# Kernel tuning notes

Hardware: AMD Instinct MI355X
Metric: run time of the kernel (lower is better)

## Reference

```python
import jax, jax.numpy as jnp
import numpy as np

N_NODES = 50000
N_EDGES = 600000
D_IN = 128
D_OUT = 128
K_HOPS = 2  # Gra_inc(2)


def _gcn_norm(edge_index, edge_weight, num_nodes, dtype):
    # Add self-loops (weight 1.0) and compute symmetric GCN normalization.
    loop = jnp.arange(num_nodes, dtype=edge_index.dtype)
    row = jnp.concatenate([edge_index[0], loop])  # source
    col = jnp.concatenate([edge_index[1], loop])  # destination
    w = jnp.concatenate([edge_weight, jnp.ones((num_nodes,), dtype=dtype)])
    deg = jax.ops.segment_sum(w, col, num_segments=num_nodes)
    dinv = jnp.where(deg > 0, jax.lax.rsqrt(deg), jnp.zeros_like(deg))
    norm = dinv[row] * w * dinv[col]  # [E + N]
    return row, col, norm


def setup_inputs() -> dict:
    key = jax.random.key(0)
    k1, k2, k3, k4 = jax.random.split(key, 4)
    x = jax.random.normal(k1, (N_NODES, D_IN), dtype=jnp.float32)
    edge_index = jax.random.randint(k2, (2, N_EDGES), 0, N_NODES, dtype=jnp.int64)
    edge_weight = jax.random.uniform(k3, (N_EDGES,), dtype=jnp.float32)
    # Linear(in,out,bias=False) weight, PyTorch layout [out, in]
    W = jax.random.normal(k4, (D_OUT, D_IN), dtype=jnp.float32) * (1.0 / np.sqrt(D_IN))
    return {"x": x, "edge_index": edge_index, "edge_weight": edge_weight, "W": W}


def reference(x, edge_index, edge_weight, W):
    num_nodes = x.shape[0]
    h = x @ W.T  # lin11: [N, D_OUT]
    row, col, norm = _gcn_norm(edge_index, edge_weight, num_nodes, h.dtype)
    # Gra_inc(2): K=2 hops of normalized sparse propagation h <- A_hat @ h
    for _ in range(K_HOPS):
        msgs = norm[:, None] * h[row]  # gather + scale, [E+N, D_OUT]
        h = jax.ops.segment_sum(msgs, col, num_segments=num_nodes)
    return h  # bias is None (bias=False)
```

## Files before the change

kernel.cpp:

```cpp
#include <hip/hip_runtime.h>

typedef unsigned long long u64;
typedef unsigned int u32;
typedef _Float16 f16;

#define NN 50000
#define NE 600000
#define D  128
#define NWAVE 3125
#define GGEMM 782
#define EPB 2048
#define NB_P 293
#define NP 196
#define MAXCAP 3584
#define NSTRIP 2
#define GS 1563

typedef __attribute__((ext_vector_type(8))) __bf16 bf16x8;
typedef __attribute__((ext_vector_type(8))) unsigned short us8;
typedef __attribute__((ext_vector_type(8))) f16 f16x8;
typedef __attribute__((ext_vector_type(4))) float f32x4;

__device__ __forceinline__ unsigned short f2bf(float f) {
    u32 u = __float_as_uint(f);
    return (unsigned short)((u + 0x7FFFu + ((u >> 16) & 1u)) >> 16);
}
__device__ __forceinline__ float bf2f(unsigned short h) {
    return __uint_as_float((u32)h << 16);
}

__global__ __launch_bounds__(256) void wprep(const float* __restrict__ W,
                                             us8* __restrict__ Whi,
                                             us8* __restrict__ Wlo,
                                             int* __restrict__ pcur) {
    const int i = blockIdx.x * 256 + threadIdx.x;
    if (i < NP) pcur[i] = i * MAXCAP;
    if (i < 2048) {
        const int ln = i & 63, nt = (i >> 6) & 7, kc4 = i >> 9;
        const float* p =
            W + (size_t)(nt * 16 + (ln & 15)) * D + kc4 * 32 + (ln >> 4) * 8;
        float v[8];
        *(float4*)&v[0] = *(const float4*)p;
        *(float4*)&v[4] = *(const float4*)(p + 4);
        us8 hi, lo;
#pragma unroll
        for (int j = 0; j < 8; ++j) {
            const unsigned short hb = f2bf(v[j]);
            hi[j] = hb;
            lo[j] = f2bf(v[j] - bf2f(hb));
        }
        Whi[i] = hi;
        Wlo[i] = lo;
    }
}

__global__ __launch_bounds__(256) void gemm_scatter(
    const float* __restrict__ x, const us8* __restrict__ Whi,
    const us8* __restrict__ Wlo, f16* __restrict__ h16,
    const int* __restrict__ row, const int* __restrict__ col,
    const float* __restrict__ w, int* __restrict__ pcur,
    u64* __restrict__ part) {
    const int t = threadIdx.x;
    __shared__ us8 WH[2048];
    __shared__ us8 WL[2048];

    if (blockIdx.x < NB_P) {
        int* bins = (int*)WH;
        int* off0 = bins + 256;
        int* cur  = off0 + 256;
        for (int i = t; i < NP; i += 256) { bins[i] = 0; cur[i] = 0; }
        __syncthreads();
        const int e0 = blockIdx.x * EPB + t;
        int cc[8];
#pragma unroll
        for (int s = 0; s < 8; ++s) {
            const int e = e0 + s * 256;
            cc[s] = (e < NE) ? col[e] : -1;
            if (cc[s] >= 0) atomicAdd(&bins[cc[s] >> 8], 1);
        }
        __syncthreads();
        for (int i = t; i < NP; i += 256)
            off0[i] = bins[i] ? atomicAdd(&pcur[i], bins[i]) : 0;
        __syncthreads();
#pragma unroll
        for (int s = 0; s < 8; ++s) {
            const int e = e0 + s * 256;
            if (e < NE) {
                const int c = cc[s];
                const int p = c >> 8;
                const int lr = atomicAdd(&cur[p], 1);
                part[off0[p] + lr] = ((u64)__float_as_uint(w[e]) << 32) |
                                     ((u32)row[e] << 8) | (u32)(c & 255);
            }
        }
        return;
    }

    const int g = (blockIdx.x - NB_P) * 4 + (t >> 6);
    const int lane = t & 63;
    const int gc = (g < NWAVE) ? g : (NWAVE - 1);
    const int row0 = gc * 16;

    const float* px = x + (size_t)(row0 + (lane & 15)) * D + (lane >> 4) * 8;
    float4 ar[8];
#pragma unroll
    for (int c = 0; c < 4; ++c) {
        ar[2 * c]     = *(const float4*)(px + c * 32);
        ar[2 * c + 1] = *(const float4*)(px + c * 32 + 4);
    }

#pragma unroll
    for (int i = 0; i < 8; ++i) {
        WH[t + i * 256] = Whi[t + i * 256];
        WL[t + i * 256] = Wlo[t + i * 256];
    }
    __syncthreads();
    if (g >= NWAVE) return;

    f32x4 acc[8];
#pragma unroll
    for (int nt = 0; nt < 8; ++nt) acc[nt] = (f32x4){0.f, 0.f, 0.f, 0.f};

#pragma unroll
    for (int c = 0; c < 4; ++c) {
        float v[8];
        *(float4*)&v[0] = ar[2 * c];
        *(float4*)&v[4] = ar[2 * c + 1];
        us8 hiu, lou;
#pragma unroll
        for (int j = 0; j < 8; ++j) {
            const unsigned short hb = f2bf(v[j]);
            hiu[j] = hb;
            lou[j] = f2bf(v[j] - bf2f(hb));
        }
        const bf16x8 ah = *(const bf16x8*)&hiu;
        const bf16x8 al = *(const bf16x8*)&lou;
#pragma unroll
        for (int nt = 0; nt < 8; ++nt) {
            const bf16x8 bh = *(const bf16x8*)&WH[c * 512 + nt * 64 + lane];
            const bf16x8 bl = *(const bf16x8*)&WL[c * 512 + nt * 64 + lane];
            acc[nt] = __builtin_amdgcn_mfma_f32_16x16x32_bf16(ah, bh, acc[nt], 0, 0, 0);
            acc[nt] = __builtin_amdgcn_mfma_f32_16x16x32_bf16(al, bh, acc[nt], 0, 0, 0);
            acc[nt] = __builtin_amdgcn_mfma_f32_16x16x32_bf16(ah, bl, acc[nt], 0, 0, 0);
        }
    }

    const int q = lane >> 4, cl = lane & 15;
#pragma unroll
    for (int nt = 0; nt < 8; ++nt) {
        f16* o = h16 + (size_t)(nt >> 2) * ((size_t)NN * 64) + (nt & 3) * 16 + cl;
#pragma unroll
        for (int r = 0; r < 4; ++r)
            o[(size_t)(row0 + q * 4 + r) * 64] = (f16)acc[nt][r];
    }
}

__global__ __launch_bounds__(256) void csr_k(
    const u64* __restrict__ part, const int* __restrict__ pcur,
    int* __restrict__ base, int* __restrict__ kcnt,
    float* __restrict__ dinv, int2* __restrict__ sedge) {
    __shared__ u32 cntL[256];
    __shared__ float wsL[256];
    __shared__ int curL[256];
    __shared__ int sw[256];
    const int p = blockIdx.x, tid = threadIdx.x;
    const int eb = p * MAXCAP, ee = pcur[p];

    cntL[tid] = 0u;
    wsL[tid] = 0.f;
    __syncthreads();
    for (int e = eb + tid; e < ee; e += 256) {
        const u64 pk = part[e];
        const int cl = (int)(pk & 255u);
        atomicAdd(&cntL[cl], 1u);
        atomicAdd(&wsL[cl], __uint_as_float((u32)(pk >> 32)));
    }
    __syncthreads();

    const int node = p * 256 + tid;
    const float di = rsqrtf(1.0f + wsL[tid]);
    const int myc = (int)cntL[tid];
    sw[tid] = myc;
    __syncthreads();
    for (int off = 1; off < 256; off <<= 1) {
        int tv = (tid >= off) ? sw[tid - off] : 0;
        __syncthreads();
        if (tid >= off) sw[tid] += tv;
        __syncthreads();
    }
    const int excl = sw[tid] - myc;
    if (node < NN) {
        dinv[node] = di;
        base[node] = eb + excl;
        kcnt[node] = myc;
    }
    __syncthreads();
    wsL[tid] = di;
    curL[tid] = excl;
    __syncthreads();

    for (int e = eb + tid; e < ee; e += 256) {
        const u64 pk = part[e];
        const int cl = (int)(pk & 255u);
        const int r = (int)((pk >> 8) & 0xFFFFu);
        const float wv = __uint_as_float((u32)(pk >> 32));
        const int lr = atomicAdd(&curL[cl], 1);
        int2 ed;
        ed.x = r;
        ed.y = __float_as_int(wv * wsL[cl]);
        sedge[eb + lr] = ed;
    }
}

template <int OUTF>
__global__ __launch_bounds__(256) void hop_kernel(
    const f16* __restrict__ src, f16* __restrict__ dst16,
    float* __restrict__ dstf, const int2* __restrict__ sedge,
    const int* __restrict__ base, const int* __restrict__ kcnt,
    const float* __restrict__ dinv) {
    const int node = blockIdx.x * 32 + (threadIdx.x >> 3);
    if (node >= NN) return;
    const int strip = blockIdx.y;
    const int lo8 = (threadIdx.x & 7) * 8;
    const f16* hs = src + (size_t)strip * ((size_t)NN * 64) + lo8;

    const int b = base[node];
    const int k = kcnt[node];

    float acc[8] = {0.f, 0.f, 0.f, 0.f, 0.f, 0.f, 0.f, 0.f};
#pragma unroll 4
    for (int j = 0; j < k; ++j) {
        const int2 ed = sedge[b + j];
        const f16x8 hv = *(const f16x8*)(hs + (size_t)ed.x * 64);
        const float nm = __int_as_float(ed.y) * dinv[ed.x];
#pragma unroll
        for (int i = 0; i < 8; ++i) acc[i] = fmaf(nm, (float)hv[i], acc[i]);
    }
    const float di = dinv[node];
    const float d2 = di * di;
    const f16x8 sv = *(const f16x8*)(hs + (size_t)node * 64);
#pragma unroll
    for (int i = 0; i < 8; ++i) acc[i] = fmaf(d2, (float)sv[i], acc[i]);

    if (OUTF) {
        float* o = dstf + (size_t)node * D + strip * 64 + lo8;
        *(float4*)&o[0] = make_float4(acc[0], acc[1], acc[2], acc[3]);
        *(float4*)&o[4] = make_float4(acc[4], acc[5], acc[6], acc[7]);
    } else {
        f16x8 ov;
#pragma unroll
        for (int i = 0; i < 8; ++i) ov[i] = (f16)acc[i];
        *(f16x8*)(dst16 + (size_t)strip * ((size_t)NN * 64) + (size_t)node * 64 + lo8) = ov;
    }
}

extern "C" void kernel_launch(void* const* d_in, const int* in_sizes, int n_in,
                              void* d_out, int out_size, void* d_ws,
                              size_t ws_size, hipStream_t stream) {
    const float* x  = (const float*)d_in[0];
    const int*   ei = (const int*)d_in[1];
    const float* w  = (const float*)d_in[2];
    const float* W  = (const float*)d_in[3];
    float* out = (float*)d_out;

    const int* row = ei;
    const int* col = ei + NE;

    f16* h16a = (f16*)d_ws;
    f16* h16b = h16a + (size_t)2 * NN * 64;
    u64* part = (u64*)h16b;
    us8* Whi = (us8*)(h16b + (size_t)2 * NN * 64);
    us8* Wlo = Whi + 2048;
    int* pcur = (int*)(Wlo + 2048);
    int* base = pcur + NP;
    int* kcnt = base + NN;
    float* dinv = (float*)(kcnt + NN);
    int2* sedge = (int2*)(dinv + NN);

    wprep<<<8, 256, 0, stream>>>(W, Whi, Wlo, pcur);
    gemm_scatter<<<NB_P + GGEMM, 256, 0, stream>>>(x, Whi, Wlo, h16a, row, col,
                                                   w, pcur, part);
    csr_k<<<NP, 256, 0, stream>>>(part, pcur, base, kcnt, dinv, sedge);

    hop_kernel<0><<<dim3(GS, NSTRIP), 256, 0, stream>>>(h16a, h16b, nullptr,
                                                        sedge, base, kcnt, dinv);
    hop_kernel<1><<<dim3(GS, NSTRIP), 256, 0, stream>>>(h16b, nullptr, out,
                                                        sedge, base, kcnt, dinv);
}
```

Before: 94.37 us.

## Make GEMM waves persistent over four row tiles with register prefetch

The GEMM part of the fused gemm/scatter kernel now launches 196 blocks instead of 782, and each wave handles four 16-row tiles strided by 784 waves. The next tile's x rows are prefetched into registers while the current tile's MFMAs run. This amortises the per-block load of W into LDS across four tiles and hides global load latency. In exchange it uses more registers, and there are fewer blocks to overlap with the scatter blocks. Overflow waves clamp to the last tile and store it redundantly.

```diff
diff --git a/kernel.cpp b/kernel.cpp
--- a/kernel.cpp
+++ b/kernel.cpp
@@ -8,7 +8,8 @@
 #define NE 600000
 #define D  128
 #define NWAVE 3125
-#define GGEMM 782
+#define GB 196
+#define GSTRIDE 784
 #define EPB 2048
 #define NB_P 293
 #define NP 196
@@ -96,12 +97,12 @@
         return;
     }
 
-    const int g = (blockIdx.x - NB_P) * 4 + (t >> 6);
+    const int wid = (blockIdx.x - NB_P) * 4 + (t >> 6);
     const int lane = t & 63;
-    const int gc = (g < NWAVE) ? g : (NWAVE - 1);
-    const int row0 = gc * 16;
-
-    const float* px = x + (size_t)(row0 + (lane & 15)) * D + (lane >> 4) * 8;
+    const int l15 = lane & 15, l4 = lane >> 4;
+
+    int g = (wid < NWAVE) ? wid : NWAVE - 1;
+    const float* px = x + (size_t)(g * 16 + l15) * D + l4 * 8;
     float4 ar[8];
 #pragma unroll
     for (int c = 0; c < 4; ++c) {
@@ -115,43 +116,62 @@
         WL[t + i * 256] = Wlo[t + i * 256];
     }
     __syncthreads();
-    if (g >= NWAVE) return;
-
-    f32x4 acc[8];
-#pragma unroll
-    for (int nt = 0; nt < 8; ++nt) acc[nt] = (f32x4){0.f, 0.f, 0.f, 0.f};
-
-#pragma unroll
-    for (int c = 0; c < 4; ++c) {
-        float v[8];
-        *(float4*)&v[0] = ar[2 * c];
-        *(float4*)&v[4] = ar[2 * c + 1];
-        us8 hiu, lou;
-#pragma unroll
-        for (int j = 0; j < 8; ++j) {
-            const unsigned short hb = f2bf(v[j]);
-            hiu[j] = hb;
-            lou[j] = f2bf(v[j] - bf2f(hb));
-        }
-        const bf16x8 ah = *(const bf16x8*)&hiu;
-        const bf16x8 al = *(const bf16x8*)&lou;
+
+#pragma unroll
+    for (int l = 0; l < 4; ++l) {
+        float4 an[8];
+        int gn = wid + (l + 1) * GSTRIDE;
+        if (gn >= NWAVE) gn = NWAVE - 1;
+        if (l < 3) {
+            const float* pn = x + (size_t)(gn * 16 + l15) * D + l4 * 8;
+#pragma unroll
+            for (int c = 0; c < 4; ++c) {
+                an[2 * c]     = *(const float4*)(pn + c * 32);
+                an[2 * c + 1] = *(const float4*)(pn + c * 32 + 4);
+            }
+        }
+
+        f32x4 acc[8];
+#pragma unroll
+        for (int nt = 0; nt < 8; ++nt) acc[nt] = (f32x4){0.f, 0.f, 0.f, 0.f};
+
+#pragma unroll
+        for (int c = 0; c < 4; ++c) {
+            float v[8];
+            *(float4*)&v[0] = ar[2 * c];
+            *(float4*)&v[4] = ar[2 * c + 1];
+            us8 hiu, lou;
+#pragma unroll
+            for (int j = 0; j < 8; ++j) {
+                const unsigned short hb = f2bf(v[j]);
+                hiu[j] = hb;
+                lou[j] = f2bf(v[j] - bf2f(hb));
+            }
+            const bf16x8 ah = *(const bf16x8*)&hiu;
+            const bf16x8 al = *(const bf16x8*)&lou;
+#pragma unroll
+            for (int nt = 0; nt < 8; ++nt) {
+                const bf16x8 bh = *(const bf16x8*)&WH[c * 512 + nt * 64 + lane];
+                const bf16x8 bl = *(const bf16x8*)&WL[c * 512 + nt * 64 + lane];
+                acc[nt] = __builtin_amdgcn_mfma_f32_16x16x32_bf16(ah, bh, acc[nt], 0, 0, 0);
+                acc[nt] = __builtin_amdgcn_mfma_f32_16x16x32_bf16(al, bh, acc[nt], 0, 0, 0);
+                acc[nt] = __builtin_amdgcn_mfma_f32_16x16x32_bf16(ah, bl, acc[nt], 0, 0, 0);
+            }
+        }
+
+        const int row0 = g * 16;
 #pragma unroll
         for (int nt = 0; nt < 8; ++nt) {
-            const bf16x8 bh = *(const bf16x8*)&WH[c * 512 + nt * 64 + lane];
-            const bf16x8 bl = *(const bf16x8*)&WL[c * 512 + nt * 64 + lane];
-            acc[nt] = __builtin_amdgcn_mfma_f32_16x16x32_bf16(ah, bh, acc[nt], 0, 0, 0);
-            acc[nt] = __builtin_amdgcn_mfma_f32_16x16x32_bf16(al, bh, acc[nt], 0, 0, 0);
-            acc[nt] = __builtin_amdgcn_mfma_f32_16x16x32_bf16(ah, bl, acc[nt], 0, 0, 0);
-        }
-    }
-
-    const int q = lane >> 4, cl = lane & 15;
-#pragma unroll
-    for (int nt = 0; nt < 8; ++nt) {
-        f16* o = h16 + (size_t)(nt >> 2) * ((size_t)NN * 64) + (nt & 3) * 16 + cl;
-#pragma unroll
-        for (int r = 0; r < 4; ++r)
-            o[(size_t)(row0 + q * 4 + r) * 64] = (f16)acc[nt][r];
+            f16* o = h16 + (size_t)(nt >> 2) * ((size_t)NN * 64) +
+                     (nt & 3) * 16 + l15;
+#pragma unroll
+            for (int r = 0; r < 4; ++r)
+                o[(size_t)(row0 + l4 * 4 + r) * 64] = (f16)acc[nt][r];
+        }
+
+        g = gn;
+#pragma unroll
+        for (int i = 0; i < 8; ++i) ar[i] = an[i];
     }
 }
 
@@ -278,8 +298,8 @@
     int2* sedge = (int2*)(dinv + NN);
 
     wprep<<<8, 256, 0, stream>>>(W, Whi, Wlo, pcur);
-    gemm_scatter<<<NB_P + GGEMM, 256, 0, stream>>>(x, Whi, Wlo, h16a, row, col,
-                                                   w, pcur, part);
+    gemm_scatter<<<NB_P + GB, 256, 0, stream>>>(x, Whi, Wlo, h16a, row, col,
+                                                w, pcur, part);
     csr_k<<<NP, 256, 0, stream>>>(part, pcur, base, kcnt, dinv, sedge);
 
     hop_kernel<0><<<dim3(GS, NSTRIP), 256, 0, stream>>>(h16a, h16b, nullptr,
```

After: 91.36 us. 1.03x faster.
